# Performance work log

Measured on AMD Instinct MI355X. Metric: run time of the kernel, lower is better.

The kernel has to match this reference:

```python
import jax, jax.numpy as jnp
import numpy as np

N = 50000      # nodes
E = 800000     # edges (before self-loops)
NFEATS = 256
NHIDS = 32
NHEADS = 8
NOUT = 128
NEG_SLOPE = 0.2


def leaky_relu(x, slope=NEG_SLOPE):
    return jnp.where(x >= 0, x, slope * x)


def gat_layer(x, src, dst, W, a_src, a_dst, b, heads, out_ch, concat):
    """PyG GATConv: h = xW; e_ij = LeakyReLU(a_s.h_j + a_d.h_i); softmax over
    edges grouped by destination; out_i = sum_j alpha_ij h_j (+bias)."""
    n = x.shape[0]
    h = (x @ W.T).reshape(n, heads, out_ch)            # [N,H,C]
    al_s = jnp.einsum('nhc,hc->nh', h, a_src)          # [N,H]
    al_d = jnp.einsum('nhc,hc->nh', h, a_dst)          # [N,H]
    e = leaky_relu(al_s[src] + al_d[dst])              # [E',H]
    e_max = jax.ops.segment_max(e, dst, num_segments=n)
    e_max = jnp.where(jnp.isfinite(e_max), e_max, 0.0)
    ex = jnp.exp(e - e_max[dst])
    denom = jax.ops.segment_sum(ex, dst, num_segments=n)
    alpha = ex / (denom[dst] + 1e-16)                  # [E',H]
    msg = h[src] * alpha[:, :, None]                   # [E',H,C]
    out = jax.ops.segment_sum(msg, dst, num_segments=n)  # [N,H,C]
    if concat:
        out = out.reshape(n, heads * out_ch)
    else:
        out = out.mean(axis=1)
    return out + b


def setup_inputs() -> dict:
    key = jax.random.key(0)
    ks = jax.random.split(key, 12)
    edge_index = jax.random.randint(ks[0], (2, E), 0, N, dtype=jnp.int64)
    x = jax.random.normal(ks[1], (N, NFEATS), dtype=jnp.float32)
    s1 = 1.0 / np.sqrt(NFEATS)
    W1 = jax.random.uniform(ks[2], (NHEADS * NHIDS, NFEATS), jnp.float32, -s1, s1)
    att_src1 = jax.random.normal(ks[3], (NHEADS, NHIDS), jnp.float32) * 0.1
    att_dst1 = jax.random.normal(ks[4], (NHEADS, NHIDS), jnp.float32) * 0.1
    b1 = jnp.zeros((NHEADS * NHIDS,), jnp.float32)
    s2 = 1.0 / np.sqrt(NHEADS * NHIDS)
    W2 = jax.random.uniform(ks[5], (NOUT, NHEADS * NHIDS), jnp.float32, -s2, s2)
    att_src2 = jax.random.normal(ks[6], (1, NOUT), jnp.float32) * 0.1
    att_dst2 = jax.random.normal(ks[7], (1, NOUT), jnp.float32) * 0.1
    b2 = jnp.zeros((NOUT,), jnp.float32)
    return {"edge_index": edge_index, "x": x,
            "W1": W1, "att_src1": att_src1, "att_dst1": att_dst1, "b1": b1,
            "W2": W2, "att_src2": att_src2, "att_dst2": att_dst2, "b2": b2}


def reference(edge_index, x, W1, att_src1, att_dst1, b1, W2, att_src2, att_dst2, b2):
    n = x.shape[0]
    loops = jnp.arange(n, dtype=edge_index.dtype)
    src = jnp.concatenate([edge_index[0], loops])  # PyG adds self-loops
    dst = jnp.concatenate([edge_index[1], loops])
    h = gat_layer(x, src, dst, W1, att_src1, att_dst1, b1, NHEADS, NHIDS, True)
    h = leaky_relu(h)  # module activation, slope 0.2
    # dropout(p=0.6, train=False) -> identity in eval mode
    out = gat_layer(h, src, dst, W2, att_src2, att_dst2, b2, 1, NOUT, True)
    return out
```

## Files before the change

kernel.cpp:

```cpp
#include <hip/hip_runtime.h>
#include <hip/hip_bf16.h>
#include <math.h>

#define NN 50000
#define EE 800000
#define ET 850000
#define NFEATS 256
#define NHIDS 32
#define NHEADS 8
#define NOUT 128

typedef __attribute__((ext_vector_type(8))) short bf16x8;
typedef __attribute__((ext_vector_type(4))) float f32x4;
typedef __attribute__((ext_vector_type(8))) unsigned short ushort8_t;

__device__ inline ushort f2bf(float x) {
    __hip_bfloat16 b = __float2bfloat16(x);
    return *reinterpret_cast<ushort*>(&b);
}
__device__ inline float bf2f(ushort u) {
    unsigned v = ((unsigned)u) << 16;
    return __builtin_bit_cast(float, v);
}
__device__ inline float bflo(unsigned u) {
    return __builtin_bit_cast(float, u << 16);
}
__device__ inline float bfhi(unsigned u) {
    return __builtin_bit_cast(float, u & 0xffff0000u);
}

__global__ void k_hist(const int* __restrict__ ei, int* __restrict__ deg) {
    int e = blockIdx.x * blockDim.x + threadIdx.x;
    if (e >= ET) return;
    int d = (e < EE) ? ei[EE + e] : (e - EE);
    atomicAdd(&deg[d], 1);
}

__global__ void k_scan_block(const int* __restrict__ deg, int* __restrict__ offsets,
                             int* __restrict__ bsum, int n) {
    __shared__ int lds[1024];
    int i = blockIdx.x * 1024 + threadIdx.x;
    int v = (i < n) ? deg[i] : 0;
    lds[threadIdx.x] = v;
    __syncthreads();
    for (int off = 1; off < 1024; off <<= 1) {
        int t = 0;
        if ((int)threadIdx.x >= off) t = lds[threadIdx.x - off];
        __syncthreads();
        lds[threadIdx.x] += t;
        __syncthreads();
    }
    if (i < n) offsets[i] = lds[threadIdx.x] - v;
    if (threadIdx.x == 1023) bsum[blockIdx.x] = lds[1023];
}

__global__ void k_scan_bsums(int* __restrict__ bsum, int nb) {
    int t = threadIdx.x;
    int v0 = (t < nb) ? bsum[t] : 0;
    int v = v0;
    for (int off = 1; off < 64; off <<= 1) {
        int u = __shfl_up(v, off, 64);
        if (t >= off) v += u;
    }
    if (t < nb) bsum[t] = v - v0;
}

__global__ void k_add_off(int* __restrict__ offsets, const int* __restrict__ bsum,
                          int n, int total) {
    int i = blockIdx.x * blockDim.x + threadIdx.x;
    if (i < n) offsets[i] += bsum[i >> 10];
    if (i == 0) offsets[n] = total;
}

__global__ void k_scatter(const int* __restrict__ ei, const int* __restrict__ offsets,
                          int* __restrict__ cursor, int* __restrict__ srcs) {
    int e = blockIdx.x * blockDim.x + threadIdx.x;
    if (e >= ET) return;
    int d, s;
    if (e < EE) { d = ei[EE + e]; s = ei[e]; }
    else        { d = e - EE;     s = e - EE; }
    int pos = offsets[d] + atomicAdd(&cursor[d], 1);
    srcs[pos] = s;
}

__global__ void k_splitW(const float* __restrict__ W, ushort* __restrict__ Wh,
                         ushort* __restrict__ Wl, int n) {
    int i = blockIdx.x * blockDim.x + threadIdx.x;
    if (i >= n) return;
    float v = W[i];
    ushort h = f2bf(v);
    Wh[i] = h;
    Wl[i] = f2bf(v - bf2f(h));
}

template <int TBN>
__global__ __launch_bounds__(512) void gemm_fused(const float* __restrict__ A,
                                                  const ushort* __restrict__ Wh,
                                                  const ushort* __restrict__ Wl,
                                                  ushort* __restrict__ Cb,
                                                  float* __restrict__ als,
                                                  float* __restrict__ ald,
                                                  const float* __restrict__ aS,
                                                  const float* __restrict__ aD,
                                                  int M) {
    constexpr int K = 256;
    constexpr int WN = TBN / 4;
    constexpr int NF = WN / 16;
    __shared__ ushort Ah[128][40], Al[128][40];
    __shared__ ushort Bh[TBN][40], Bl[TBN][40];
    __shared__ float att_red[256];

    int tid = threadIdx.x;
    int wid = tid >> 6, lane = tid & 63;
    int wm = wid >> 2, wn = wid & 3;
    int m0 = blockIdx.x * 128;

    f32x4 acc[4][NF];
#pragma unroll
    for (int i = 0; i < 4; i++)
#pragma unroll
        for (int j = 0; j < NF; j++) acc[i][j] = (f32x4){0.f, 0.f, 0.f, 0.f};

    for (int k0 = 0; k0 < K; k0 += 32) {
#pragma unroll
        for (int i = 0; i < 2; i++) {
            int s = tid + 512 * i;
            int r = s >> 3, c4 = s & 7;
            float4 v = make_float4(0.f, 0.f, 0.f, 0.f);
            if (m0 + r < M) v = *(const float4*)(A + (size_t)(m0 + r) * K + k0 + c4 * 4);
            ushort4 hi, lo;
            hi.x = f2bf(v.x); lo.x = f2bf(v.x - bf2f(hi.x));
            hi.y = f2bf(v.y); lo.y = f2bf(v.y - bf2f(hi.y));
            hi.z = f2bf(v.z); lo.z = f2bf(v.z - bf2f(hi.z));
            hi.w = f2bf(v.w); lo.w = f2bf(v.w - bf2f(hi.w));
            *(ushort4*)&Ah[r][c4 * 4] = hi;
            *(ushort4*)&Al[r][c4 * 4] = lo;
        }
        if constexpr (TBN == 256) {
            int r = tid >> 1, c16 = (tid & 1) * 16;
            const ushort* gh = Wh + (size_t)r * K + k0 + c16;
            const ushort* gl = Wl + (size_t)r * K + k0 + c16;
            *(ushort8_t*)&Bh[r][c16]     = *(const ushort8_t*)gh;
            *(ushort8_t*)&Bh[r][c16 + 8] = *(const ushort8_t*)(gh + 8);
            *(ushort8_t*)&Bl[r][c16]     = *(const ushort8_t*)gl;
            *(ushort8_t*)&Bl[r][c16 + 8] = *(const ushort8_t*)(gl + 8);
        } else {
            int s = tid & 255;
            int r = s >> 1, c16 = (s & 1) * 16;
            const ushort* gp = ((tid < 256) ? Wh : Wl) + (size_t)r * K + k0 + c16;
            ushort* lp = ((tid < 256) ? &Bh[r][c16] : &Bl[r][c16]);
            *(ushort8_t*)lp       = *(const ushort8_t*)gp;
            *(ushort8_t*)(lp + 8) = *(const ushort8_t*)(gp + 8);
        }
        __syncthreads();

        int koff = (lane >> 4) * 8;
        int rsel = lane & 15;
        bf16x8 ah[4], al[4], bh[NF], bl[NF];
#pragma unroll
        for (int mf = 0; mf < 4; mf++) {
            int r = wm * 64 + mf * 16 + rsel;
            ah[mf] = *(const bf16x8*)&Ah[r][koff];
            al[mf] = *(const bf16x8*)&Al[r][koff];
        }
#pragma unroll
        for (int nf = 0; nf < NF; nf++) {
            int c = wn * WN + nf * 16 + rsel;
            bh[nf] = *(const bf16x8*)&Bh[c][koff];
            bl[nf] = *(const bf16x8*)&Bl[c][koff];
        }
#pragma unroll
        for (int mf = 0; mf < 4; mf++)
#pragma unroll
            for (int nf = 0; nf < NF; nf++) {
                acc[mf][nf] = __builtin_amdgcn_mfma_f32_16x16x32_bf16(ah[mf], bh[nf], acc[mf][nf], 0, 0, 0);
                acc[mf][nf] = __builtin_amdgcn_mfma_f32_16x16x32_bf16(ah[mf], bl[nf], acc[mf][nf], 0, 0, 0);
                acc[mf][nf] = __builtin_amdgcn_mfma_f32_16x16x32_bf16(al[mf], bh[nf], acc[mf][nf], 0, 0, 0);
            }
        __syncthreads();
    }

    int l15 = lane & 15, lhi = lane >> 4;

#pragma unroll
    for (int mf = 0; mf < 4; mf++) {
        int gr0 = m0 + wm * 64 + mf * 16 + lhi * 4;
#pragma unroll
        for (int nf = 0; nf < NF; nf++) {
            int gc = wn * WN + nf * 16 + l15;
#pragma unroll
            for (int j = 0; j < 4; j++)
                if (gr0 + j < M) Cb[(size_t)(gr0 + j) * TBN + gc] = f2bf(acc[mf][nf][j]);
        }
    }

    if constexpr (TBN == 256) {
        float as0 = aS[wn * 64 + l15],      as0b = aS[wn * 64 + 16 + l15];
        float as1 = aS[wn * 64 + 32 + l15], as1b = aS[wn * 64 + 48 + l15];
        float ad0 = aD[wn * 64 + l15],      ad0b = aD[wn * 64 + 16 + l15];
        float ad1 = aD[wn * 64 + 32 + l15], ad1b = aD[wn * 64 + 48 + l15];
#pragma unroll
        for (int mf = 0; mf < 4; mf++) {
#pragma unroll
            for (int j = 0; j < 4; j++) {
                float ps0 = acc[mf][0][j] * as0 + acc[mf][1][j] * as0b;
                float ps1 = acc[mf][2][j] * as1 + acc[mf][3][j] * as1b;
                float pd0 = acc[mf][0][j] * ad0 + acc[mf][1][j] * ad0b;
                float pd1 = acc[mf][2][j] * ad1 + acc[mf][3][j] * ad1b;
#pragma unroll
                for (int off = 1; off <= 8; off <<= 1) {
                    ps0 += __shfl_xor(ps0, off, 64);
                    ps1 += __shfl_xor(ps1, off, 64);
                    pd0 += __shfl_xor(pd0, off, 64);
                    pd1 += __shfl_xor(pd1, off, 64);
                }
                int gr = m0 + wm * 64 + mf * 16 + lhi * 4 + j;
                if (l15 == 0 && gr < M) {
                    als[gr * 8 + 2 * wn]     = ps0;
                    als[gr * 8 + 2 * wn + 1] = ps1;
                    ald[gr * 8 + 2 * wn]     = pd0;
                    ald[gr * 8 + 2 * wn + 1] = pd1;
                }
            }
        }
    } else {
        float asv0 = aS[wn * 32 + l15], asv1 = aS[wn * 32 + 16 + l15];
        float adv0 = aD[wn * 32 + l15], adv1 = aD[wn * 32 + 16 + l15];
        if (tid < 256) att_red[tid] = 0.f;
        __syncthreads();
#pragma unroll
        for (int mf = 0; mf < 4; mf++) {
#pragma unroll
            for (int j = 0; j < 4; j++) {
                float ps = acc[mf][0][j] * asv0 + acc[mf][1][j] * asv1;
                float pd = acc[mf][0][j] * adv0 + acc[mf][1][j] * adv1;
#pragma unroll
                for (int off = 1; off <= 8; off <<= 1) {
                    ps += __shfl_xor(ps, off, 64);
                    pd += __shfl_xor(pd, off, 64);
                }
                if (l15 == 0) {
                    int rl = wm * 64 + mf * 16 + lhi * 4 + j;
                    atomicAdd(&att_red[rl], ps);
                    atomicAdd(&att_red[128 + rl], pd);
                }
            }
        }
        __syncthreads();
        if (tid < 128 && m0 + tid < M) {
            als[m0 + tid] = att_red[tid];
            ald[m0 + tid] = att_red[128 + tid];
        }
    }
}

__global__ __launch_bounds__(128) void k_agg1(
    const ushort* __restrict__ h1b, const float* __restrict__ als,
    const float* __restrict__ ald, const int* __restrict__ offsets,
    const int* __restrict__ srcs, const float* __restrict__ b1,
    float* __restrict__ out1) {
    int n = blockIdx.x;
    int tid = threadIdx.x;
    int lane = tid & 63;
    int wv = tid >> 6;
    int hl = lane >> 4;
    int base = offsets[n], deg = offsets[n + 1] - base;

    int eL = lane >> 2;
    int hS = wv * 4 + (lane & 3);
    float aldS = ald[n * 8 + hS];

    float acc0 = 0.f, acc1 = 0.f, dsum = 0.f;
    int chunk = 0;
    for (; chunk + 16 <= deg; chunk += 16) {
        int sE = srcs[base + chunk + eL];
        float v = als[sE * 8 + hS] + aldS;
        v = (v >= 0.f) ? v : 0.2f * v;
        float wE = __expf(v);
#pragma unroll
        for (int i = 0; i < 16; i++) {
            int si = __shfl(sE, i * 4, 64);
            float wi = __shfl(wE, i * 4 + hl, 64);
            unsigned u = *(const unsigned*)(h1b + (size_t)si * 256 + 2 * tid);
            acc0 += wi * bflo(u);
            acc1 += wi * bfhi(u);
            dsum += wi;
        }
    }
    if (chunk < deg) {
        int len = deg - chunk;
        int idx = chunk + eL; if (idx >= deg) idx = deg - 1;
        int sE = srcs[base + idx];
        float v = als[sE * 8 + hS] + aldS;
        v = (v >= 0.f) ? v : 0.2f * v;
        float wE = __expf(v);
        for (int i = 0; i < len; i++) {
            int si = __shfl(sE, i * 4, 64);
            float wi = __shfl(wE, i * 4 + hl, 64);
            unsigned u = *(const unsigned*)(h1b + (size_t)si * 256 + 2 * tid);
            acc0 += wi * bflo(u);
            acc1 += wi * bfhi(u);
            dsum += wi;
        }
    }
    float inv = 1.f / (dsum + 1e-16f);
    float r0 = acc0 * inv + b1[2 * tid];
    float r1 = acc1 * inv + b1[2 * tid + 1];
    r0 = (r0 >= 0.f) ? r0 : 0.2f * r0;
    r1 = (r1 >= 0.f) ? r1 : 0.2f * r1;
    *(float2*)(out1 + (size_t)n * 256 + 2 * tid) = make_float2(r0, r1);
}

__global__ __launch_bounds__(64) void k_agg2(
    const ushort* __restrict__ h2b, const float* __restrict__ als,
    const float* __restrict__ ald, const int* __restrict__ offsets,
    const int* __restrict__ srcs, const float* __restrict__ b2,
    float* __restrict__ out) {
    int n = blockIdx.x;
    int lane = threadIdx.x;
    int l16 = lane & 15;
    int base = offsets[n], deg = offsets[n + 1] - base;
    float aldv = ald[n];

    float acc0 = 0.f, acc1 = 0.f, dsum = 0.f;
    int chunk = 0;
    for (; chunk + 16 <= deg; chunk += 16) {
        int sE = srcs[base + chunk + l16];
        float v = als[sE] + aldv;
        v = (v >= 0.f) ? v : 0.2f * v;
        float wE = __expf(v);
#pragma unroll
        for (int i = 0; i < 16; i++) {
            int si = __shfl(sE, i, 64);
            float wi = __shfl(wE, i, 64);
            unsigned u = *(const unsigned*)(h2b + (size_t)si * 128 + 2 * lane);
            acc0 += wi * bflo(u);
            acc1 += wi * bfhi(u);
            dsum += wi;
        }
    }
    if (chunk < deg) {
        int len = deg - chunk;
        int idx = chunk + l16; if (idx >= deg) idx = deg - 1;
        int sE = srcs[base + idx];
        float v = als[sE] + aldv;
        v = (v >= 0.f) ? v : 0.2f * v;
        float wE = __expf(v);
        for (int i = 0; i < len; i++) {
            int si = __shfl(sE, i, 64);
            float wi = __shfl(wE, i, 64);
            unsigned u = *(const unsigned*)(h2b + (size_t)si * 128 + 2 * lane);
            acc0 += wi * bflo(u);
            acc1 += wi * bfhi(u);
            dsum += wi;
        }
    }
    float inv = 1.f / (dsum + 1e-16f);
    *(float2*)(out + (size_t)n * 128 + 2 * lane) =
        make_float2(acc0 * inv + b2[2 * lane], acc1 * inv + b2[2 * lane + 1]);
}

extern "C" void kernel_launch(void* const* d_in, const int* in_sizes, int n_in,
                              void* d_out, int out_size, void* d_ws, size_t ws_size,
                              hipStream_t stream) {
    const int* ei = (const int*)d_in[0];
    const float* x = (const float*)d_in[1];
    const float* W1 = (const float*)d_in[2];
    const float* aS1 = (const float*)d_in[3];
    const float* aD1 = (const float*)d_in[4];
    const float* b1 = (const float*)d_in[5];
    const float* W2 = (const float*)d_in[6];
    const float* aS2 = (const float*)d_in[7];
    const float* aD2 = (const float*)d_in[8];
    const float* b2 = (const float*)d_in[9];
    float* out = (float*)d_out;

    char* w = (char*)d_ws;
    auto alloc = [&](size_t bytes) {
        char* p = w;
        w += (bytes + 255) & ~(size_t)255;
        return p;
    };
    ushort* h1b  = (ushort*)alloc((size_t)NN * 256 * 2);
    float*  out1 = (float*)alloc((size_t)NN * 256 * 4);
    float*  als1 = (float*)alloc((size_t)NN * 8 * 4);
    float*  ald1 = (float*)alloc((size_t)NN * 8 * 4);
    int* deg     = (int*)alloc((size_t)(NN + 1) * 4);
    int* offsets = (int*)alloc((size_t)(NN + 1) * 4);
    int* cursor  = (int*)alloc((size_t)NN * 4);
    int* srcs    = (int*)alloc((size_t)ET * 4);
    int* bsum    = (int*)alloc(64 * 4);
    ushort* W1h  = (ushort*)alloc((size_t)256 * 256 * 2);
    ushort* W1l  = (ushort*)alloc((size_t)256 * 256 * 2);
    ushort* W2h  = (ushort*)alloc((size_t)128 * 256 * 2);
    ushort* W2l  = (ushort*)alloc((size_t)128 * 256 * 2);
    ushort* h2b = h1b;
    float* als2 = als1;
    float* ald2 = ald1;

    const int nb = (NN + 1023) / 1024;

    hipMemsetAsync(deg, 0, (size_t)NN * 4, stream);
    hipMemsetAsync(cursor, 0, (size_t)NN * 4, stream);

    k_splitW<<<(256 * 256 + 255) / 256, 256, 0, stream>>>(W1, W1h, W1l, 256 * 256);
    k_splitW<<<(128 * 256 + 255) / 256, 256, 0, stream>>>(W2, W2h, W2l, 128 * 256);

    k_hist<<<(ET + 255) / 256, 256, 0, stream>>>(ei, deg);
    k_scan_block<<<nb, 1024, 0, stream>>>(deg, offsets, bsum, NN);
    k_scan_bsums<<<1, 64, 0, stream>>>(bsum, nb);
    k_add_off<<<(NN + 255) / 256, 256, 0, stream>>>(offsets, bsum, NN, ET);
    k_scatter<<<(ET + 255) / 256, 256, 0, stream>>>(ei, offsets, cursor, srcs);

    gemm_fused<256><<<(NN + 127) / 128, 512, 0, stream>>>(x, W1h, W1l, h1b, als1, ald1, aS1, aD1, NN);
    k_agg1<<<NN, 128, 0, stream>>>(h1b, als1, ald1, offsets, srcs, b1, out1);

    gemm_fused<128><<<(NN + 127) / 128, 512, 0, stream>>>(out1, W2h, W2l, h2b, als2, ald2, aS2, aD2, NN);
    k_agg2<<<NN, 64, 0, stream>>>(h2b, als2, ald2, offsets, srcs, b2, out);
}
```

Measured before the change: 294.2 us.

## Use one wavefront per node with 16-byte gathers in GAT aggregation kernels

Both aggregation kernels now process one destination node per 64-lane wavefront, two nodes per block. Each lane gathers 8 bf16 features with a single uint4 load, so several edges are processed in parallel across lane groups and combined at the end with a cross-lane shuffle reduction. The full-chunk and tail loops are merged into one loop that zeroes the weights of out-of-range edges. The aim is wider, fewer memory transactions and more edge-level parallelism, at the cost of more registers and wasted lanes on low-degree tails.

```diff
diff --git a/kernel.cpp b/kernel.cpp
--- a/kernel.cpp
+++ b/kernel.cpp
@@ -259,105 +259,119 @@
     const float* __restrict__ ald, const int* __restrict__ offsets,
     const int* __restrict__ srcs, const float* __restrict__ b1,
     float* __restrict__ out1) {
-    int n = blockIdx.x;
-    int tid = threadIdx.x;
-    int lane = tid & 63;
-    int wv = tid >> 6;
-    int hl = lane >> 4;
+    int lane = threadIdx.x & 63;
+    int wv = threadIdx.x >> 6;
+    int n = blockIdx.x * 2 + wv;
+    int g = lane >> 5;
+    int c32 = lane & 31;
+    int head = c32 >> 2;
     int base = offsets[n], deg = offsets[n + 1] - base;
 
-    int eL = lane >> 2;
-    int hS = wv * 4 + (lane & 3);
+    int eL8 = lane >> 3;
+    int hS = lane & 7;
     float aldS = ald[n * 8 + hS];
 
-    float acc0 = 0.f, acc1 = 0.f, dsum = 0.f;
-    int chunk = 0;
-    for (; chunk + 16 <= deg; chunk += 16) {
-        int sE = srcs[base + chunk + eL];
-        float v = als[sE * 8 + hS] + aldS;
-        v = (v >= 0.f) ? v : 0.2f * v;
-        float wE = __expf(v);
-#pragma unroll
-        for (int i = 0; i < 16; i++) {
-            int si = __shfl(sE, i * 4, 64);
-            float wi = __shfl(wE, i * 4 + hl, 64);
-            unsigned u = *(const unsigned*)(h1b + (size_t)si * 256 + 2 * tid);
-            acc0 += wi * bflo(u);
-            acc1 += wi * bfhi(u);
+    float acc[8] = {0.f, 0.f, 0.f, 0.f, 0.f, 0.f, 0.f, 0.f};
+    float dsum = 0.f;
+    for (int chunk = 0; chunk < deg; chunk += 16) {
+        int len = deg - chunk; if (len > 16) len = 16;
+        int i0 = chunk + eL8;     if (i0 >= deg) i0 = deg - 1;
+        int i1 = chunk + 8 + eL8; if (i1 >= deg) i1 = deg - 1;
+        int sE0 = srcs[base + i0];
+        int sE1 = srcs[base + i1];
+        float v0 = als[sE0 * 8 + hS] + aldS;
+        float v1 = als[sE1 * 8 + hS] + aldS;
+        v0 = (v0 >= 0.f) ? v0 : 0.2f * v0;
+        v1 = (v1 >= 0.f) ? v1 : 0.2f * v1;
+        float w0 = __expf(v0), w1 = __expf(v1);
+#pragma unroll
+        for (int i = 0; i < 8; i++) {
+            int e = 2 * i + g;
+            int slot = (e & 7) * 8;
+            int si = __shfl((i < 4) ? sE0 : sE1, slot, 64);
+            float wi = __shfl((i < 4) ? w0 : w1, slot + head, 64);
+            if (e >= len) wi = 0.f;
+            uint4 hv = *(const uint4*)(h1b + (size_t)si * 256 + 8 * c32);
+            acc[0] += wi * bflo(hv.x); acc[1] += wi * bfhi(hv.x);
+            acc[2] += wi * bflo(hv.y); acc[3] += wi * bfhi(hv.y);
+            acc[4] += wi * bflo(hv.z); acc[5] += wi * bfhi(hv.z);
+            acc[6] += wi * bflo(hv.w); acc[7] += wi * bfhi(hv.w);
             dsum += wi;
         }
     }
-    if (chunk < deg) {
-        int len = deg - chunk;
-        int idx = chunk + eL; if (idx >= deg) idx = deg - 1;
-        int sE = srcs[base + idx];
-        float v = als[sE * 8 + hS] + aldS;
-        v = (v >= 0.f) ? v : 0.2f * v;
-        float wE = __expf(v);
-        for (int i = 0; i < len; i++) {
-            int si = __shfl(sE, i * 4, 64);
-            float wi = __shfl(wE, i * 4 + hl, 64);
-            unsigned u = *(const unsigned*)(h1b + (size_t)si * 256 + 2 * tid);
-            acc0 += wi * bflo(u);
-            acc1 += wi * bfhi(u);
-            dsum += wi;
-        }
-    }
-    float inv = 1.f / (dsum + 1e-16f);
-    float r0 = acc0 * inv + b1[2 * tid];
-    float r1 = acc1 * inv + b1[2 * tid + 1];
-    r0 = (r0 >= 0.f) ? r0 : 0.2f * r0;
-    r1 = (r1 >= 0.f) ? r1 : 0.2f * r1;
-    *(float2*)(out1 + (size_t)n * 256 + 2 * tid) = make_float2(r0, r1);
-}
-
-__global__ __launch_bounds__(64) void k_agg2(
+#pragma unroll
+    for (int j = 0; j < 8; j++) acc[j] += __shfl_xor(acc[j], 32, 64);
+    dsum += __shfl_xor(dsum, 32, 64);
+
+    if (g == 0) {
+        float inv = 1.f / (dsum + 1e-16f);
+        const float* bb = b1 + 8 * c32;
+        float r[8];
+#pragma unroll
+        for (int j = 0; j < 8; j++) {
+            float t = acc[j] * inv + bb[j];
+            r[j] = (t >= 0.f) ? t : 0.2f * t;
+        }
+        float* o = out1 + (size_t)n * 256 + 8 * c32;
+        *(float4*)o       = make_float4(r[0], r[1], r[2], r[3]);
+        *(float4*)(o + 4) = make_float4(r[4], r[5], r[6], r[7]);
+    }
+}
+
+__global__ __launch_bounds__(128) void k_agg2(
     const ushort* __restrict__ h2b, const float* __restrict__ als,
     const float* __restrict__ ald, const int* __restrict__ offsets,
     const int* __restrict__ srcs, const float* __restrict__ b2,
     float* __restrict__ out) {
-    int n = blockIdx.x;
-    int lane = threadIdx.x;
-    int l16 = lane & 15;
+    int lane = threadIdx.x & 63;
+    int wv = threadIdx.x >> 6;
+    int n = blockIdx.x * 2 + wv;
+    int g = lane >> 4;
+    int c16 = lane & 15;
     int base = offsets[n], deg = offsets[n + 1] - base;
     float aldv = ald[n];
 
-    float acc0 = 0.f, acc1 = 0.f, dsum = 0.f;
-    int chunk = 0;
-    for (; chunk + 16 <= deg; chunk += 16) {
-        int sE = srcs[base + chunk + l16];
-        float v = als[sE] + aldv;
-        v = (v >= 0.f) ? v : 0.2f * v;
-        float wE = __expf(v);
-#pragma unroll
-        for (int i = 0; i < 16; i++) {
-            int si = __shfl(sE, i, 64);
-            float wi = __shfl(wE, i, 64);
-            unsigned u = *(const unsigned*)(h2b + (size_t)si * 128 + 2 * lane);
-            acc0 += wi * bflo(u);
-            acc1 += wi * bfhi(u);
-            dsum += wi;
-        }
-    }
-    if (chunk < deg) {
-        int len = deg - chunk;
-        int idx = chunk + l16; if (idx >= deg) idx = deg - 1;
+    float acc[8] = {0.f, 0.f, 0.f, 0.f, 0.f, 0.f, 0.f, 0.f};
+    float dsum = 0.f;
+    for (int chunk = 0; chunk < deg; chunk += 16) {
+        int len = deg - chunk; if (len > 16) len = 16;
+        int idx = chunk + c16; if (idx >= deg) idx = deg - 1;
         int sE = srcs[base + idx];
         float v = als[sE] + aldv;
         v = (v >= 0.f) ? v : 0.2f * v;
         float wE = __expf(v);
-        for (int i = 0; i < len; i++) {
-            int si = __shfl(sE, i, 64);
-            float wi = __shfl(wE, i, 64);
-            unsigned u = *(const unsigned*)(h2b + (size_t)si * 128 + 2 * lane);
-            acc0 += wi * bflo(u);
-            acc1 += wi * bfhi(u);
+#pragma unroll
+        for (int i = 0; i < 4; i++) {
+            int e = 4 * i + g;
+            int si = __shfl(sE, e, 64);
+            float wi = __shfl(wE, e, 64);
+            if (e >= len) wi = 0.f;
+            uint4 hv = *(const uint4*)(h2b + (size_t)si * 128 + 8 * c16);
+            acc[0] += wi * bflo(hv.x); acc[1] += wi * bfhi(hv.x);
+            acc[2] += wi * bflo(hv.y); acc[3] += wi * bfhi(hv.y);
+            acc[4] += wi * bflo(hv.z); acc[5] += wi * bfhi(hv.z);
+            acc[6] += wi * bflo(hv.w); acc[7] += wi * bfhi(hv.w);
             dsum += wi;
         }
     }
-    float inv = 1.f / (dsum + 1e-16f);
-    *(float2*)(out + (size_t)n * 128 + 2 * lane) =
-        make_float2(acc0 * inv + b2[2 * lane], acc1 * inv + b2[2 * lane + 1]);
+#pragma unroll
+    for (int j = 0; j < 8; j++) {
+        acc[j] += __shfl_xor(acc[j], 16, 64);
+        acc[j] += __shfl_xor(acc[j], 32, 64);
+    }
+    dsum += __shfl_xor(dsum, 16, 64);
+    dsum += __shfl_xor(dsum, 32, 64);
+
+    if (g == 0) {
+        float inv = 1.f / (dsum + 1e-16f);
+        const float* bb = b2 + 8 * c16;
+        float r[8];
+#pragma unroll
+        for (int j = 0; j < 8; j++) r[j] = acc[j] * inv + bb[j];
+        float* o = out + (size_t)n * 128 + 8 * c16;
+        *(float4*)o       = make_float4(r[0], r[1], r[2], r[3]);
+        *(float4*)(o + 4) = make_float4(r[4], r[5], r[6], r[7]);
+    }
 }
 
 extern "C" void kernel_launch(void* const* d_in, const int* in_sizes, int n_in,
@@ -413,8 +427,8 @@
     k_scatter<<<(ET + 255) / 256, 256, 0, stream>>>(ei, offsets, cursor, srcs);
 
     gemm_fused<256><<<(NN + 127) / 128, 512, 0, stream>>>(x, W1h, W1l, h1b, als1, ald1, aS1, aD1, NN);
-    k_agg1<<<NN, 128, 0, stream>>>(h1b, als1, ald1, offsets, srcs, b1, out1);
+    k_agg1<<<NN / 2, 128, 0, stream>>>(h1b, als1, ald1, offsets, srcs, b1, out1);
 
     gemm_fused<128><<<(NN + 127) / 128, 512, 0, stream>>>(out1, W2h, W2l, h2b, als2, ald2, aS2, aD2, NN);
-    k_agg2<<<NN, 64, 0, stream>>>(h2b, als2, ald2, offsets, srcs, b2, out);
-}
+    k_agg2<<<NN / 2, 128, 0, stream>>>(h2b, als2, ald2, offsets, srcs, b2, out);
+}
```

Result: faster. 271.3 us (-7.8%).
